# Performance work log

Hardware: AMD Instinct MI355X
Metric: run time of the kernel (lower is better)

The kernel has to match this reference:

```python
import jax, jax.numpy as jnp
import numpy as np
from jax import lax

H = 256  # hidden_dim
NDIM = 3
K = 32   # k_neighbors


def sincos_embed(coords, dim, ndim):
    # ContinuousSinCosEmbed: per-coordinate sin/cos features, zero-padded to `dim`.
    dpn = dim // ndim          # channels per coordinate
    half = dpn // 2
    freqs = 1.0 / (10000.0 ** (jnp.arange(half, dtype=coords.dtype) / half))
    ang = coords[..., :, None] * freqs                      # (..., ndim, half)
    emb = jnp.concatenate([jnp.sin(ang), jnp.cos(ang)], -1)  # (..., ndim, 2*half)
    emb = emb.reshape(coords.shape[:-1] + (ndim * 2 * half,))
    pad = dim - ndim * 2 * half
    if pad:
        emb = jnp.concatenate([emb, jnp.zeros(emb.shape[:-1] + (pad,), emb.dtype)], -1)
    return emb


def setup_inputs() -> dict:
    key = jax.random.key(0)
    ks = jax.random.split(key, 8)
    N, S = 50000, 1024
    positions = jax.random.uniform(ks[0], (N, NDIM), dtype=jnp.float32) * 10.0
    supernode_indices = jax.random.randint(ks[1], (S,), 0, N, dtype=jnp.int32)
    g = 1.0 / np.sqrt(H)
    W1 = jax.random.normal(ks[2], (H, H), jnp.float32) * g
    b1 = jnp.zeros((H,), jnp.float32)
    W2 = jax.random.normal(ks[3], (H, H), jnp.float32) * g
    b2 = jnp.zeros((H,), jnp.float32)
    Wp = jax.random.normal(ks[4], (2 * H, H), jnp.float32) * (1.0 / np.sqrt(2 * H))
    bp = jnp.zeros((H,), jnp.float32)
    return {"positions": positions, "supernode_indices": supernode_indices,
            "W1": W1, "b1": b1, "W2": W2, "b2": b2, "Wp": Wp, "bp": bp}


def reference(positions, supernode_indices, W1, b1, W2, b2, Wp, bp):
    # positions: (N, 3); supernode_indices: (S,)
    sup_pos = positions[supernode_indices]                 # (S, 3)
    # kNN neighbor search via dense pairwise squared distances (memory-bound)
    diff = sup_pos[:, None, :] - positions[None, :, :]     # (S, N, 3)
    dist2 = jnp.sum(diff * diff, axis=-1)                  # (S, N)
    _, nbr_idx = lax.top_k(-dist2, K)                      # (S, K)
    nbr_pos = positions[nbr_idx]                           # (S, K, 3)
    # relpos mode: embed (relative position, distance) -> ndim+1 = 4 coords
    rel = sup_pos[:, None, :] - nbr_pos                    # (S, K, 3)
    d = jnp.sqrt(jnp.sum(rel * rel, axis=-1, keepdims=True))  # (S, K, 1)
    rel_feat = jnp.concatenate([rel, d], axis=-1)          # (S, K, 4)
    msg_in = sincos_embed(rel_feat, H, NDIM + 1)           # (S, K, H)
    # message MLP: Dense -> gelu -> Dense
    h = jax.nn.gelu(jnp.einsum('ski,ij->skj', msg_in, W1) + b1)
    msgs = jnp.einsum('ski,ij->skj', h, W2) + b2           # (S, K, H)
    # scatter-reduce: mean over neighbors per supernode
    agg = jnp.mean(msgs, axis=1)                           # (S, H)
    # supernode absolute position embedding, concat, project
    sup_emb = sincos_embed(sup_pos, H, NDIM)               # (S, H)
    feats = jnp.concatenate([sup_emb, agg], axis=-1)       # (S, 2H)
    out = feats @ Wp + bp                                  # (S, H)
    return out[None]                                        # (1, S, H)
```

## Files before the change

### kernel.cpp

```cpp
#include <hip/hip_runtime.h>
#include <hip/hip_bf16.h>
#include <math.h>

typedef short bf16x8 __attribute__((ext_vector_type(8)));
typedef float f32x4  __attribute__((ext_vector_type(4)));

constexpr int   H     = 256;
constexpr int   KNB   = 32;
constexpr int   TPB   = 512;
constexpr int   GC    = 16;
constexpr float HINV  = 1.6f;
constexpr float HCEL  = 0.625f;
constexpr int   SLOTS = 32;
constexpr int   OCAP  = 256;
constexpr int   CAP   = 512;

__device__ __forceinline__ ushort f2bf(float x) {
    unsigned u = __float_as_uint(x);
    u += 0x7FFF + ((u >> 16) & 1);
    return (ushort)(u >> 16);
}

__device__ __forceinline__ float bf2f(ushort u) {
    return __uint_as_float(((unsigned)u) << 16);
}

__device__ __forceinline__ float gelu_fast(float x) {
    float u = 0.7978845608028654f * (x + 0.044715f * x * x * x);
    float t = exp2f(-2.885390081777927f * u);
    return x / (1.0f + t);
}

__device__ __forceinline__ int cell_of(float x, float y, float z) {
    int cx = min(GC - 1, max(0, (int)(x * HINV)));
    int cy = min(GC - 1, max(0, (int)(y * HINV)));
    int cz = min(GC - 1, max(0, (int)(z * HINV)));
    return (cz * GC + cy) * GC + cx;
}

__global__ __launch_bounds__(256)
void prep(const float* __restrict__ W1, const float* __restrict__ Wp,
          const float* __restrict__ W2, const float* __restrict__ pos, int N,
          ushort* __restrict__ W1t, ushort* __restrict__ Wpt,
          ushort* __restrict__ W2b, float4* __restrict__ pos4s,
          int* __restrict__ origidx, int* __restrict__ cellcnt,
          int* __restrict__ ovfidx, float4* __restrict__ ovfpos) {
    const int b = blockIdx.x;
    if (b < 64) {
        __shared__ float tile[32][33];
        const int ti = b >> 3, tj = b & 7;
        const int r  = threadIdx.x >> 5, c = threadIdx.x & 31;
#pragma unroll
        for (int rr = r; rr < 32; rr += 8)
            tile[rr][c] = W1[(ti * 32 + rr) * H + tj * 32 + c];
        __syncthreads();
#pragma unroll
        for (int rr = r; rr < 32; rr += 8)
            W1t[(tj * 32 + rr) * H + ti * 32 + c] = f2bf(tile[c][rr]);
    } else if (b < 192) {
        __shared__ float tile[32][33];
        const int b2 = b - 64;
        const int ti = b2 >> 3, tj = b2 & 7;
        const int r  = threadIdx.x >> 5, c = threadIdx.x & 31;
#pragma unroll
        for (int rr = r; rr < 32; rr += 8)
            tile[rr][c] = Wp[(ti * 32 + rr) * H + tj * 32 + c];
        __syncthreads();
#pragma unroll
        for (int rr = r; rr < 32; rr += 8)
            Wpt[(tj * 32 + rr) * (2 * H) + ti * 32 + c] = f2bf(tile[c][rr]);
    } else if (b < 256) {
        const int e4 = (b - 192) * 1024 + threadIdx.x * 4;
        float4 v = *(const float4*)&W2[e4];
        ushort4 o;
        o.x = f2bf(v.x); o.y = f2bf(v.y); o.z = f2bf(v.z); o.w = f2bf(v.w);
        *(ushort4*)&W2b[e4] = o;
    } else {
        int i = (b - 256) * 256 + threadIdx.x;
        if (i < N) {
            float x = pos[3 * i], y = pos[3 * i + 1], z = pos[3 * i + 2];
            float4 P = make_float4(x, y, z, 0.f);
            int c = cell_of(x, y, z);
            int slot = atomicAdd(&cellcnt[c], 1);
            if (slot < SLOTS) {
                pos4s[c * SLOTS + slot] = P;
                origidx[c * SLOTS + slot] = i;
            } else {
                int o = atomicAdd(&cellcnt[4096], 1);
                if (o < OCAP) { ovfpos[o] = P; ovfidx[o] = i; }
            }
        }
    }
}

__global__ __launch_bounds__(TPB, 8)
void fused_knn_mlp(const float* __restrict__ pos,
                   const float4* __restrict__ pos4s,
                   const int* __restrict__ origidx,
                   const int* __restrict__ cellcnt,
                   const int* __restrict__ ovfidx, const float4* __restrict__ ovfpos,
                   const int* __restrict__ supidx,
                   const ushort* __restrict__ W1t, const float* __restrict__ b1,
                   const ushort* __restrict__ W2b, const float* __restrict__ b2,
                   ushort* __restrict__ featsB)
{
    __shared__ __align__(16) char pool[16384];
    float* amaxd = (float*)pool;
    int*   acnt  = (int*)(pool + 512);
    int*   ccell = (int*)(pool + 1024);
    int*   ccnt  = (int*)(pool + 2048);
    float* cmnd  = (float*)(pool + 3072);
    int*   cpre  = (int*)(pool + 4096);
    float* d2buf = (float*)(pool + 5120);
    int*   obuf  = (int*)(pool + 7168);
    float* pxb   = (float*)(pool + 9216);
    float* pyb   = (float*)(pool + 11264);
    float* pzb   = (float*)(pool + 13312);
    ushort* msg  = (ushort*)pool;
    float*  p2   = (float*)pool;

    __shared__ float rf[KNB][5];
    __shared__ int   selo[KNB];
    __shared__ float hb[H];
    __shared__ int   wsum[4];
    __shared__ float tau2_sh, tau32_sh;
    __shared__ int   cnt_sh, ncl;

    const int s    = blockIdx.x;
    const int t    = threadIdx.x;
    const int lane = t & 63;
    const int w    = t >> 6;

    const int sidx = supidx[s];
    const float sx = pos[3 * sidx], sy = pos[3 * sidx + 1], sz = pos[3 * sidx + 2];

    constexpr float L2_10000 = 13.287712379549449f;

    if (t == 0) { ncl = 0; tau2_sh = 301.f; }

    const int scx = min(GC - 1, max(0, (int)(sx * HINV)));
    const int scy = min(GC - 1, max(0, (int)(sy * HINV)));
    const int scz = min(GC - 1, max(0, (int)(sz * HINV)));
    const int ax0 = max(0, scx - 2), ax1 = min(GC - 1, scx + 2);
    const int ay0 = max(0, scy - 2), ay1 = min(GC - 1, scy + 2);
    const int az0 = max(0, scz - 2), az1 = min(GC - 1, scz + 2);
    const int anx = ax1 - ax0 + 1, any_ = ay1 - ay0 + 1, anz = az1 - az0 + 1;
    const int an  = anx * any_ * anz;
    if (t < an) {
        int ci = t;
        int X = ax0 + ci % anx, rem = ci / anx;
        int Y = ay0 + rem % any_, Z = az0 + rem / any_;
        int cell = (Z * GC + Y) * GC + X;
        acnt[ci] = min(cellcnt[cell], SLOTS);
        float lx = X * HCEL, ly = Y * HCEL, lz = Z * HCEL;
        float mx = fmaxf(fabsf(sx - lx), fabsf(lx + HCEL - sx));
        float my = fmaxf(fabsf(sy - ly), fabsf(ly + HCEL - sy));
        float mz = fmaxf(fabsf(sz - lz), fabsf(lz + HCEL - sz));
        amaxd[ci] = mx * mx + my * my + mz * mz;
    }

    if (t < 256) {
        float se = 0.f;
        if (t < 252) {
            int c  = t / 84;
            int rr = t - c * 84;
            int f  = (rr < 42) ? rr : rr - 42;
            float coord = (c == 0) ? sx : ((c == 1) ? sy : sz);
            float ang = coord * exp2f(-(float)f * (L2_10000 / 42.f));
            se = (rr < 42) ? __sinf(ang) : __cosf(ang);
        }
        featsB[s * (2 * H) + t] = f2bf(se);
    }
    __syncthreads();
    if (t < an) {
        int ci = t;
        float myv = amaxd[ci];
        int Sc = 0;
        for (int j = 0; j < an; j++) {
            bool less = (amaxd[j] < myv) || (amaxd[j] == myv && j < ci);
            Sc += less ? acnt[j] : 0;
        }
        if (Sc < KNB && KNB <= Sc + acnt[ci]) tau2_sh = myv;
    }
    __syncthreads();
    const float tau2 = tau2_sh;
    const float R2 = tau2 + 1e-3f;
    const float R  = sqrtf(R2);
    if (t == 0) tau32_sh = R2;

    const int bx0 = max(0, (int)floorf((sx - R) * HINV));
    const int bx1 = min(GC - 1, (int)floorf((sx + R) * HINV));
    const int by0 = max(0, (int)floorf((sy - R) * HINV));
    const int by1 = min(GC - 1, (int)floorf((sy + R) * HINV));
    const int bz0 = max(0, (int)floorf((sz - R) * HINV));
    const int bz1 = min(GC - 1, (int)floorf((sz + R) * HINV));
    const bool inwin = (bx0 >= ax0 && bx1 <= ax1 && by0 >= ay0 && by1 <= ay1 &&
                        bz0 >= az0 && bz1 <= az1);
    if (inwin) {
        if (t < an) {
            int ci = t;
            int cn = acnt[ci];
            if (cn > 0) {
                int X = ax0 + ci % anx, rem = ci / anx;
                int Y = ay0 + rem % any_, Z = az0 + rem / any_;
                float lx = X * HCEL, ly = Y * HCEL, lz = Z * HCEL;
                float ddx = fmaxf(fmaxf(lx - sx, sx - (lx + HCEL)), 0.f);
                float ddy = fmaxf(fmaxf(ly - sy, sy - (ly + HCEL)), 0.f);
                float ddz = fmaxf(fmaxf(lz - sz, sz - (lz + HCEL)), 0.f);
                float mnd = ddx * ddx + ddy * ddy + ddz * ddz;
                if (mnd <= R2) {
                    int p1 = (amaxd[ci] <= tau2) ? 1 : 0;
                    int cell = (Z * GC + Y) * GC + X;
                    int sl = atomicAdd(&ncl, 1);
                    if (sl < 256) { ccell[sl] = cell; ccnt[sl] = cn | (p1 << 8); cmnd[sl] = mnd; }
                }
            }
        }
    } else {
        const int nbx = bx1 - bx0 + 1, nby = by1 - by0 + 1, nbz = bz1 - bz0 + 1;
        const int ncb = nbx * nby * nbz;
        for (int ci = t; ci < ncb; ci += TPB) {
            int X = bx0 + ci % nbx, rem = ci / nbx;
            int Y = by0 + rem % nby, Z = bz0 + rem / nby;
            float lx = X * HCEL, ly = Y * HCEL, lz = Z * HCEL;
            float ddx = fmaxf(fmaxf(lx - sx, sx - (lx + HCEL)), 0.f);
            float ddy = fmaxf(fmaxf(ly - sy, sy - (ly + HCEL)), 0.f);
            float ddz = fmaxf(fmaxf(lz - sz, sz - (lz + HCEL)), 0.f);
            float mnd = ddx * ddx + ddy * ddy + ddz * ddz;
            if (mnd > R2) continue;
            int cell = (Z * GC + Y) * GC + X;
            int cn = min(cellcnt[cell], SLOTS);
            if (cn == 0) continue;
            float mx = fmaxf(fabsf(sx - lx), fabsf(lx + HCEL - sx));
            float my = fmaxf(fabsf(sy - ly), fabsf(ly + HCEL - sy));
            float mz = fmaxf(fabsf(sz - lz), fabsf(lz + HCEL - sz));
            float amx = mx * mx + my * my + mz * mz;
            int p1 = (amx <= tau2) ? 1 : 0;
            int sl = atomicAdd(&ncl, 1);
            if (sl < 256) { ccell[sl] = cell; ccnt[sl] = cn | (p1 << 8); cmnd[sl] = mnd; }
        }
    }
    __syncthreads();
    const int nclc = min(ncl, 256);

    auto build_prefix = [&](int phase, float tlim) -> int {
        int v = 0;
        if (t < 256) {
            if (t < nclc) {
                int cc = ccnt[t];
                int cn = cc & 0xff;
                int p1 = cc >> 8;
                v = (phase == 1) ? (p1 ? cn : 0)
                                 : ((!p1 && cmnd[t] <= tlim) ? cn : 0);
            }
#pragma unroll
            for (int off = 1; off < 64; off <<= 1) {
                int x = __shfl_up(v, off);
                if (lane >= off) v += x;
            }
            if (lane == 63) wsum[w] = v;
        }
        __syncthreads();
        if (t < 256) {
            int add = 0;
#pragma unroll
            for (int j = 0; j < 4; j++) if (j < w) add += wsum[j];
            cpre[t] = v + add;
        }
        __syncthreads();
        return cpre[255];
    };
    auto bsearch = [&](int j) -> int {
        int lo = 0;
#pragma unroll
        for (int st = 128; st; st >>= 1) {
            int nlo = lo + st;
            if (nlo <= 256 && cpre[nlo - 1] <= j) lo = nlo;
        }
        return lo;
    };

    const int tot1 = build_prefix(1, 0.f);
    const int M1 = min(tot1, CAP);
    if (t < M1) {
        int j = t;
        int lo = bsearch(j);
        int off = j - (lo ? cpre[lo - 1] : 0);
        int u = ccell[lo] * SLOTS + off;
        float4 P = pos4s[u];
        float dx = sx - P.x, dy = sy - P.y, dz = sz - P.z;
        d2buf[j] = dx * dx + dy * dy + dz * dz;
        obuf[j]  = origidx[u];
        pxb[j] = P.x; pyb[j] = P.y; pzb[j] = P.z;
    }
    const int Mp1 = (M1 + 3) & ~3;
    if (M1 + t < Mp1) { d2buf[M1 + t] = INFINITY; obuf[M1 + t] = 0x7fffffff; }
    if (t == 0) cnt_sh = M1;
    __syncthreads();

    if (t < M1) {
        int u = t;
        float myv = d2buf[u];
        int   myo = obuf[u];
        int rank = 0;
        for (int v2 = 0; v2 < Mp1; v2 += 4) {
            float4 dv = *(const float4*)&d2buf[v2];
            int4   iv = *(const int4*)&obuf[v2];
            rank += (dv.x < myv) || (dv.x == myv && iv.x < myo);
            rank += (dv.y < myv) || (dv.y == myv && iv.y < myo);
            rank += (dv.z < myv) || (dv.z == myv && iv.z < myo);
            rank += (dv.w < myv) || (dv.w == myv && iv.w < myo);
        }
        if (rank == KNB - 1) tau32_sh = myv;
    }
    __syncthreads();
    const float tau32 = tau32_sh;

    const int tot2 = build_prefix(2, tau32);
    for (int j0 = 0; j0 < tot2; j0 += TPB) {
        int j = j0 + t;
        bool pass = false; float pd2 = 0.f; int po = 0; float qx = 0, qy = 0, qz = 0;
        if (j < tot2) {
            int lo = bsearch(j);
            int off = j - (lo ? cpre[lo - 1] : 0);
            int u = ccell[lo] * SLOTS + off;
            float4 P = pos4s[u];
            float dx = sx - P.x, dy = sy - P.y, dz = sz - P.z;
            pd2 = dx * dx + dy * dy + dz * dz;
            if (pd2 <= tau32) { pass = true; po = origidx[u]; qx = P.x; qy = P.y; qz = P.z; }
        }
        unsigned long long m = __ballot(pass);
        if (m) {
            int ldr = __ffsll(m) - 1;
            int base = 0;
            if (lane == ldr) base = atomicAdd(&cnt_sh, __popcll(m));
            base = __shfl(base, ldr);
            if (pass) {
                int slp = base + __popcll(m & ((1ull << lane) - 1ull));
                if (slp < CAP) {
                    d2buf[slp] = pd2; obuf[slp] = po;
                    pxb[slp] = qx; pyb[slp] = qy; pzb[slp] = qz;
                }
            }
        }
    }
    {
        int no = min(cellcnt[4096], OCAP);
        for (int j = t; j < no; j += TPB) {
            float4 P = ovfpos[j];
            float dx = sx - P.x, dy = sy - P.y, dz = sz - P.z;
            float pd2 = dx * dx + dy * dy + dz * dz;
            if (pd2 <= tau32) {
                int slp = atomicAdd(&cnt_sh, 1);
                if (slp < CAP) {
                    d2buf[slp] = pd2; obuf[slp] = ovfidx[j];
                    pxb[slp] = P.x; pyb[slp] = P.y; pzb[slp] = P.z;
                }
            }
        }
    }
    __syncthreads();
    const int M = min(cnt_sh, CAP);
    const int Mpad = (M + 3) & ~3;
    if (M + t < Mpad) { d2buf[M + t] = INFINITY; obuf[M + t] = 0x7fffffff; }
    __syncthreads();

    if (t < M) {
        int u = t;
        float myv = d2buf[u];
        int   myo = obuf[u];
        int rank = 0;
        for (int v2 = 0; v2 < Mpad; v2 += 4) {
            float4 dv = *(const float4*)&d2buf[v2];
            int4   iv = *(const int4*)&obuf[v2];
            rank += (dv.x < myv) || (dv.x == myv && iv.x < myo);
            rank += (dv.y < myv) || (dv.y == myv && iv.y < myo);
            rank += (dv.z < myv) || (dv.z == myv && iv.z < myo);
            rank += (dv.w < myv) || (dv.w == myv && iv.w < myo);
        }
        if (rank < KNB) selo[rank] = u;
    }
    __syncthreads();
    if (t < KNB) {
        int u = selo[t];
        float rx = sx - pxb[u], ry = sy - pyb[u], rz = sz - pzb[u];
        float dd = sqrtf(d2buf[u]);
        rf[t][0] = rx; rf[t][1] = ry; rf[t][2] = rz; rf[t][3] = dd;
    }
    __syncthreads();

#pragma unroll
    for (int n = 0; n < 8; n++) {
        int item = t + n * TPB;
        int f = item & 31;
        int c = (item >> 5) & 3;
        int k = item >> 7;
        float ang = rf[k][c] * exp2f(-(float)f * (L2_10000 / 32.f));
        int swz = (k & 7) << 3;
        msg[((k << 8) | (c * 64 + f))      ^ swz] = f2bf(__sinf(ang));
        msg[((k << 8) | (c * 64 + 32 + f)) ^ swz] = f2bf(__cosf(ang));
    }
    __syncthreads();

    {
        const int lr = lane & 15;
        const int lg = lane >> 4;
        f32x4 acc00 = {0,0,0,0}, acc01 = {0,0,0,0};
        f32x4 acc10 = {0,0,0,0}, acc11 = {0,0,0,0};
#pragma unroll
        for (int kk = 0; kk < 8; kk++) {
            const int i0 = kk * 32 + lg * 8;
            bf16x8 a0 = *(const bf16x8*)(W1t + ((32 * w      + lr) << 8) + i0);
            bf16x8 a1 = *(const bf16x8*)(W1t + ((32 * w + 16 + lr) << 8) + i0);
            const int swz = (lr & 7) << 3;
            bf16x8 b0  = *(const bf16x8*)(msg + ((( lr       << 8) | i0) ^ swz));
            bf16x8 b1v = *(const bf16x8*)(msg + ((((lr + 16) << 8) | i0) ^ swz));
            acc00 = __builtin_amdgcn_mfma_f32_16x16x32_bf16(a0, b0,  acc00, 0, 0, 0);
            acc01 = __builtin_amdgcn_mfma_f32_16x16x32_bf16(a0, b1v, acc01, 0, 0, 0);
            acc10 = __builtin_amdgcn_mfma_f32_16x16x32_bf16(a1, b0,  acc10, 0, 0, 0);
            acc11 = __builtin_amdgcn_mfma_f32_16x16x32_bf16(a1, b1v, acc11, 0, 0, 0);
        }
        float part[8];
#pragma unroll
        for (int mm = 0; mm < 2; mm++)
#pragma unroll
            for (int r = 0; r < 4; r++) {
                int j = 32 * w + 16 * mm + 4 * lg + r;
                float bj = b1[j];
                float h0 = (mm == 0 ? acc00[r] : acc10[r]) + bj;
                float h1 = (mm == 0 ? acc01[r] : acc11[r]) + bj;
                part[mm * 4 + r] = gelu_fast(h0) + gelu_fast(h1);
            }
#pragma unroll
        for (int off = 1; off < 16; off <<= 1)
#pragma unroll
            for (int u = 0; u < 8; u++)
                part[u] += __shfl_xor(part[u], off);
        if (lr == 0) {
#pragma unroll
            for (int u = 0; u < 8; u++) {
                int mm = u >> 2, r = u & 3;
                hb[32 * w + 16 * mm + 4 * lg + r] = part[u] * (1.0f / 32.0f);
            }
        }
    }
    __syncthreads();

    {
        const int j4 = lane * 4;
        const int ib = w * 32;
        float4 a = {0.f, 0.f, 0.f, 0.f};
#pragma unroll 4
        for (int i = 0; i < 32; i++) {
            float hv = hb[ib + i];
            ushort4 wv = *(const ushort4*)&W2b[(ib + i) * H + j4];
            a.x = fmaf(hv, bf2f(wv.x), a.x);
            a.y = fmaf(hv, bf2f(wv.y), a.y);
            a.z = fmaf(hv, bf2f(wv.z), a.z);
            a.w = fmaf(hv, bf2f(wv.w), a.w);
        }
        *(float4*)&p2[w * 256 + j4] = a;
    }
    __syncthreads();
    if (t < 256) {
        float agg = b2[t];
#pragma unroll
        for (int g = 0; g < 8; g++) agg += p2[g * 256 + t];
        featsB[s * (2 * H) + H + t] = f2bf(agg);
    }
}

__global__ __launch_bounds__(512)
void mfma_out(const ushort* __restrict__ featsB, const ushort* __restrict__ Wpt,
              const float* __restrict__ bp, float* __restrict__ out)
{
    const int bm   = blockIdx.x;
    const int t    = threadIdx.x;
    const int lane = t & 63;
    const int w    = t >> 6;
    const int lr   = lane & 15;
    const int lg   = lane >> 4;

    f32x4 acc[2][2];
#pragma unroll
    for (int mt = 0; mt < 2; mt++)
#pragma unroll
        for (int nt = 0; nt < 2; nt++) acc[mt][nt] = (f32x4){0, 0, 0, 0};

#pragma unroll
    for (int kk = 0; kk < 16; kk++) {
        const int i0 = kk * 32 + lg * 8;
        bf16x8 a0 = *(const bf16x8*)(featsB + (32 * bm      + lr) * 512 + i0);
        bf16x8 a1 = *(const bf16x8*)(featsB + (32 * bm + 16 + lr) * 512 + i0);
        bf16x8 b0 = *(const bf16x8*)(Wpt + (32 * w      + lr) * 512 + i0);
        bf16x8 b1 = *(const bf16x8*)(Wpt + (32 * w + 16 + lr) * 512 + i0);
        acc[0][0] = __builtin_amdgcn_mfma_f32_16x16x32_bf16(a0, b0, acc[0][0], 0, 0, 0);
        acc[0][1] = __builtin_amdgcn_mfma_f32_16x16x32_bf16(a0, b1, acc[0][1], 0, 0, 0);
        acc[1][0] = __builtin_amdgcn_mfma_f32_16x16x32_bf16(a1, b0, acc[1][0], 0, 0, 0);
        acc[1][1] = __builtin_amdgcn_mfma_f32_16x16x32_bf16(a1, b1, acc[1][1], 0, 0, 0);
    }
#pragma unroll
    for (int mt = 0; mt < 2; mt++)
#pragma unroll
        for (int nt = 0; nt < 2; nt++)
#pragma unroll
            for (int r = 0; r < 4; r++) {
                int srow = 32 * bm + 16 * mt + 4 * lg + r;
                int j    = 32 * w  + 16 * nt + lr;
                out[srow * H + j] = acc[mt][nt][r] + bp[j];
            }
}

extern "C" void kernel_launch(void* const* d_in, const int* in_sizes, int n_in,
                              void* d_out, int out_size, void* d_ws, size_t ws_size,
                              hipStream_t stream) {
    const float* pos = (const float*)d_in[0];
    const int*   sup = (const int*)d_in[1];
    const float* W1  = (const float*)d_in[2];
    const float* b1  = (const float*)d_in[3];
    const float* W2  = (const float*)d_in[4];
    const float* b2  = (const float*)d_in[5];
    const float* Wp  = (const float*)d_in[6];
    const float* bp  = (const float*)d_in[7];

    const int N = in_sizes[0] / 3;
    const int S = in_sizes[1];
    float* out = (float*)d_out;

    char* ws = (char*)d_ws;
    ushort* W1t     = (ushort*)ws;
    ushort* Wpt     = (ushort*)(ws + (128 << 10));
    ushort* W2b     = (ushort*)(ws + (384 << 10));
    float4* pos4s   = (float4*)(ws + (512 << 10));
    int*    origidx = (int*)(ws + (2560 << 10));
    int*    cellcnt = (int*)(ws + (3072 << 10));
    int*    ovfidx  = (int*)(ws + (3092 << 10));
    float4* ovfpos  = (float4*)(ws + (3096 << 10));
    ushort* featsB  = (ushort*)(ws + (3104 << 10));

    hipMemsetAsync(cellcnt, 0, 4097 * sizeof(int), stream);
    prep<<<256 + (N + 255) / 256, 256, 0, stream>>>(W1, Wp, W2, pos, N,
                                                    W1t, Wpt, W2b, pos4s,
                                                    origidx, cellcnt, ovfidx, ovfpos);
    fused_knn_mlp<<<S, TPB, 0, stream>>>(pos, pos4s, origidx, cellcnt,
                                         ovfidx, ovfpos, sup,
                                         W1t, b1, W2b, b2, featsB);
    mfma_out<<<S / 32, 512, 0, stream>>>(featsB, Wpt, bp, out);
}
```

Baseline: 80.93 us.

## Move W2 projection out of per-supernode kernel into batched MFMA output GEMM

The per-supernode second-layer matvec (mean hidden times W2), previously done with scalar FMAs in the fused kNN kernel, is moved into the output kernel as a batched bf16 MFMA GEMM over 16 supernodes per block. Its result goes through swizzled shared memory and is then multiplied by Wp. This relies on linearity: the mean of the messages equals the mean hidden vector times W2. W2 is now transposed in prep, and the point-scatter blocks each read 1024 positions with vectorized float4 loads. The fused kernel loses two syncs and a shared buffer, but the output kernel does more work per block and the aggregate is rounded to bf16 an extra time.

Result: faster. 76.95 us (median of 2 runs) (-4.9%).

```diff
diff --git a/kernel.cpp b/kernel.cpp
--- a/kernel.cpp
+++ b/kernel.cpp
@@ -21,10 +21,6 @@
     return (ushort)(u >> 16);
 }
 
-__device__ __forceinline__ float bf2f(ushort u) {
-    return __uint_as_float(((unsigned)u) << 16);
-}
-
 __device__ __forceinline__ float gelu_fast(float x) {
     float u = 0.7978845608028654f * (x + 0.044715f * x * x * x);
     float t = exp2f(-2.885390081777927f * u);
@@ -42,7 +38,7 @@
 void prep(const float* __restrict__ W1, const float* __restrict__ Wp,
           const float* __restrict__ W2, const float* __restrict__ pos, int N,
           ushort* __restrict__ W1t, ushort* __restrict__ Wpt,
-          ushort* __restrict__ W2b, float4* __restrict__ pos4s,
+          ushort* __restrict__ W2t, float4* __restrict__ pos4s,
           int* __restrict__ origidx, int* __restrict__ cellcnt,
           int* __restrict__ ovfidx, float4* __restrict__ ovfpos) {
     const int b = blockIdx.x;
@@ -70,15 +66,22 @@
         for (int rr = r; rr < 32; rr += 8)
             Wpt[(tj * 32 + rr) * (2 * H) + ti * 32 + c] = f2bf(tile[c][rr]);
     } else if (b < 256) {
-        const int e4 = (b - 192) * 1024 + threadIdx.x * 4;
-        float4 v = *(const float4*)&W2[e4];
-        ushort4 o;
-        o.x = f2bf(v.x); o.y = f2bf(v.y); o.z = f2bf(v.z); o.w = f2bf(v.w);
-        *(ushort4*)&W2b[e4] = o;
+        __shared__ float tile[32][33];
+        const int b2 = b - 192;
+        const int ti = b2 >> 3, tj = b2 & 7;
+        const int r  = threadIdx.x >> 5, c = threadIdx.x & 31;
+#pragma unroll
+        for (int rr = r; rr < 32; rr += 8)
+            tile[rr][c] = W2[(ti * 32 + rr) * H + tj * 32 + c];
+        __syncthreads();
+#pragma unroll
+        for (int rr = r; rr < 32; rr += 8)
+            W2t[(tj * 32 + rr) * H + ti * 32 + c] = f2bf(tile[c][rr]);
     } else {
-        int i = (b - 256) * 256 + threadIdx.x;
-        if (i < N) {
-            float x = pos[3 * i], y = pos[3 * i + 1], z = pos[3 * i + 2];
+        const int sb = b - 256;
+        const int base = sb * 1024;
+        const int t = threadIdx.x;
+        auto scat = [&](float x, float y, float z, int i) {
             float4 P = make_float4(x, y, z, 0.f);
             int c = cell_of(x, y, z);
             int slot = atomicAdd(&cellcnt[c], 1);
@@ -89,6 +92,20 @@
                 int o = atomicAdd(&cellcnt[4096], 1);
                 if (o < OCAP) { ovfpos[o] = P; ovfidx[o] = i; }
             }
+        };
+        if (base + 1024 <= N) {
+            const float4* p4 = (const float4*)(pos + (size_t)base * 3);
+            float4 f0 = p4[3 * t + 0];
+            float4 f1 = p4[3 * t + 1];
+            float4 f2 = p4[3 * t + 2];
+            const int ib = base + 4 * t;
+            scat(f0.x, f0.y, f0.z, ib + 0);
+            scat(f0.w, f1.x, f1.y, ib + 1);
+            scat(f1.z, f1.w, f2.x, ib + 2);
+            scat(f2.y, f2.z, f2.w, ib + 3);
+        } else {
+            for (int i = base + t; i < N; i += 256)
+                scat(pos[3 * i], pos[3 * i + 1], pos[3 * i + 2], i);
         }
     }
 }
@@ -101,8 +118,7 @@
                    const int* __restrict__ ovfidx, const float4* __restrict__ ovfpos,
                    const int* __restrict__ supidx,
                    const ushort* __restrict__ W1t, const float* __restrict__ b1,
-                   const ushort* __restrict__ W2b, const float* __restrict__ b2,
-                   ushort* __restrict__ featsB)
+                   ushort* __restrict__ supEB, ushort* __restrict__ hbB)
 {
     __shared__ __align__(16) char pool[16384];
     float* amaxd = (float*)pool;
@@ -117,11 +133,9 @@
     float* pyb   = (float*)(pool + 11264);
     float* pzb   = (float*)(pool + 13312);
     ushort* msg  = (ushort*)pool;
-    float*  p2   = (float*)pool;
 
     __shared__ float rf[KNB][5];
     __shared__ int   selo[KNB];
-    __shared__ float hb[H];
     __shared__ int   wsum[4];
     __shared__ float tau2_sh, tau32_sh;
     __shared__ int   cnt_sh, ncl;
@@ -169,7 +183,7 @@
             float ang = coord * exp2f(-(float)f * (L2_10000 / 42.f));
             se = (rr < 42) ? __sinf(ang) : __cosf(ang);
         }
-        featsB[s * (2 * H) + t] = f2bf(se);
+        supEB[s * H + t] = f2bf(se);
     }
     __syncthreads();
     if (t < an) {
@@ -440,40 +454,19 @@
 #pragma unroll
             for (int u = 0; u < 8; u++) {
                 int mm = u >> 2, r = u & 3;
-                hb[32 * w + 16 * mm + 4 * lg + r] = part[u] * (1.0f / 32.0f);
-            }
-        }
-    }
-    __syncthreads();
-
-    {
-        const int j4 = lane * 4;
-        const int ib = w * 32;
-        float4 a = {0.f, 0.f, 0.f, 0.f};
-#pragma unroll 4
-        for (int i = 0; i < 32; i++) {
-            float hv = hb[ib + i];
-            ushort4 wv = *(const ushort4*)&W2b[(ib + i) * H + j4];
-            a.x = fmaf(hv, bf2f(wv.x), a.x);
-            a.y = fmaf(hv, bf2f(wv.y), a.y);
-            a.z = fmaf(hv, bf2f(wv.z), a.z);
-            a.w = fmaf(hv, bf2f(wv.w), a.w);
-        }
-        *(float4*)&p2[w * 256 + j4] = a;
-    }
-    __syncthreads();
-    if (t < 256) {
-        float agg = b2[t];
-#pragma unroll
-        for (int g = 0; g < 8; g++) agg += p2[g * 256 + t];
-        featsB[s * (2 * H) + H + t] = f2bf(agg);
+                hbB[s * H + 32 * w + 16 * mm + 4 * lg + r] = f2bf(part[u] * (1.0f / 32.0f));
+            }
+        }
     }
 }
 
 __global__ __launch_bounds__(512)
-void mfma_out(const ushort* __restrict__ featsB, const ushort* __restrict__ Wpt,
-              const float* __restrict__ bp, float* __restrict__ out)
+void mfma_out2(const ushort* __restrict__ hbB, const ushort* __restrict__ supEB,
+               const ushort* __restrict__ W2t, const float* __restrict__ b2,
+               const ushort* __restrict__ Wpt, const float* __restrict__ bp,
+               float* __restrict__ out)
 {
+    __shared__ ushort agg[16 * 256];
     const int bm   = blockIdx.x;
     const int t    = threadIdx.x;
     const int lane = t & 63;
@@ -481,34 +474,51 @@
     const int lr   = lane & 15;
     const int lg   = lane >> 4;
 
-    f32x4 acc[2][2];
+    f32x4 acc1[2] = {{0,0,0,0},{0,0,0,0}};
+#pragma unroll
+    for (int kk = 0; kk < 8; kk++) {
+        const int i0 = kk * 32 + lg * 8;
+        bf16x8 bf = *(const bf16x8*)(hbB + (16 * bm + lr) * H + i0);
+        bf16x8 a0 = *(const bf16x8*)(W2t + ((32 * w      + lr) << 8) + i0);
+        bf16x8 a1 = *(const bf16x8*)(W2t + ((32 * w + 16 + lr) << 8) + i0);
+        acc1[0] = __builtin_amdgcn_mfma_f32_16x16x32_bf16(a0, bf, acc1[0], 0, 0, 0);
+        acc1[1] = __builtin_amdgcn_mfma_f32_16x16x32_bf16(a1, bf, acc1[1], 0, 0, 0);
+    }
 #pragma unroll
     for (int mt = 0; mt < 2; mt++)
 #pragma unroll
-        for (int nt = 0; nt < 2; nt++) acc[mt][nt] = (f32x4){0, 0, 0, 0};
-
+        for (int r = 0; r < 4; r++) {
+            int j = 32 * w + 16 * mt + 4 * lg + r;
+            int sl = lane & 15;
+            float v = acc1[mt][r] + b2[j];
+            agg[((sl << 8) | j) ^ ((sl & 7) << 3)] = f2bf(v);
+        }
+    __syncthreads();
+
+    f32x4 acc2[2] = {{0,0,0,0},{0,0,0,0}};
 #pragma unroll
     for (int kk = 0; kk < 16; kk++) {
-        const int i0 = kk * 32 + lg * 8;
-        bf16x8 a0 = *(const bf16x8*)(featsB + (32 * bm      + lr) * 512 + i0);
-        bf16x8 a1 = *(const bf16x8*)(featsB + (32 * bm + 16 + lr) * 512 + i0);
-        bf16x8 b0 = *(const bf16x8*)(Wpt + (32 * w      + lr) * 512 + i0);
-        bf16x8 b1 = *(const bf16x8*)(Wpt + (32 * w + 16 + lr) * 512 + i0);
-        acc[0][0] = __builtin_amdgcn_mfma_f32_16x16x32_bf16(a0, b0, acc[0][0], 0, 0, 0);
-        acc[0][1] = __builtin_amdgcn_mfma_f32_16x16x32_bf16(a0, b1, acc[0][1], 0, 0, 0);
-        acc[1][0] = __builtin_amdgcn_mfma_f32_16x16x32_bf16(a1, b0, acc[1][0], 0, 0, 0);
-        acc[1][1] = __builtin_amdgcn_mfma_f32_16x16x32_bf16(a1, b1, acc[1][1], 0, 0, 0);
+        const int io = kk * 32 + lg * 8;
+        bf16x8 bf;
+        if (kk < 8) {
+            bf = *(const bf16x8*)(supEB + (16 * bm + lr) * H + io);
+        } else {
+            int c = io - 256;
+            bf = *(const bf16x8*)(agg + (((lr << 8) | c) ^ ((lr & 7) << 3)));
+        }
+        bf16x8 a0 = *(const bf16x8*)(Wpt + (32 * w      + lr) * 512 + io);
+        bf16x8 a1 = *(const bf16x8*)(Wpt + (32 * w + 16 + lr) * 512 + io);
+        acc2[0] = __builtin_amdgcn_mfma_f32_16x16x32_bf16(a0, bf, acc2[0], 0, 0, 0);
+        acc2[1] = __builtin_amdgcn_mfma_f32_16x16x32_bf16(a1, bf, acc2[1], 0, 0, 0);
     }
 #pragma unroll
     for (int mt = 0; mt < 2; mt++)
 #pragma unroll
-        for (int nt = 0; nt < 2; nt++)
-#pragma unroll
-            for (int r = 0; r < 4; r++) {
-                int srow = 32 * bm + 16 * mt + 4 * lg + r;
-                int j    = 32 * w  + 16 * nt + lr;
-                out[srow * H + j] = acc[mt][nt][r] + bp[j];
-            }
+        for (int r = 0; r < 4; r++) {
+            int jo = 32 * w + 16 * mt + 4 * lg + r;
+            int srow = 16 * bm + (lane & 15);
+            out[srow * H + jo] = acc2[mt][r] + bp[jo];
+        }
 }
 
 extern "C" void kernel_launch(void* const* d_in, const int* in_sizes, int n_in,
@@ -530,20 +540,22 @@
     char* ws = (char*)d_ws;
     ushort* W1t     = (ushort*)ws;
     ushort* Wpt     = (ushort*)(ws + (128 << 10));
-    ushort* W2b     = (ushort*)(ws + (384 << 10));
+    ushort* W2t     = (ushort*)(ws + (384 << 10));
     float4* pos4s   = (float4*)(ws + (512 << 10));
     int*    origidx = (int*)(ws + (2560 << 10));
     int*    cellcnt = (int*)(ws + (3072 << 10));
     int*    ovfidx  = (int*)(ws + (3092 << 10));
     float4* ovfpos  = (float4*)(ws + (3096 << 10));
-    ushort* featsB  = (ushort*)(ws + (3104 << 10));
+    ushort* supEB   = (ushort*)(ws + (3104 << 10));
+    ushort* hbB     = (ushort*)(ws + (3616 << 10));
 
     hipMemsetAsync(cellcnt, 0, 4097 * sizeof(int), stream);
-    prep<<<256 + (N + 255) / 256, 256, 0, stream>>>(W1, Wp, W2, pos, N,
-                                                    W1t, Wpt, W2b, pos4s,
-                                                    origidx, cellcnt, ovfidx, ovfpos);
+    const int nscat = (N + 1023) / 1024;
+    prep<<<256 + nscat, 256, 0, stream>>>(W1, Wp, W2, pos, N,
+                                          W1t, Wpt, W2t, pos4s,
+                                          origidx, cellcnt, ovfidx, ovfpos);
     fused_knn_mlp<<<S, TPB, 0, stream>>>(pos, pos4s, origidx, cellcnt,
                                          ovfidx, ovfpos, sup,
-                                         W1t, b1, W2b, b2, featsB);
-    mfma_out<<<S / 32, 512, 0, stream>>>(featsB, Wpt, bp, out);
-}
+                                         W1t, b1, supEB, hbB);
+    mfma_out2<<<S / 16, 512, 0, stream>>>(hbB, supEB, W2t, b2, Wpt, bp, out);
+}
```
